# Kernel optimization log

Hardware: AMD Instinct MI355X
Metric: run time of the kernel (lower is better)

The kernel has to match this reference:

```python
import jax, jax.numpy as jnp
import numpy as np

B = 128
GRID = (256, 256)
N = GRID[0] * GRID[1]
P = 1024          # number of persistence pairs per sample (fixed for jit)
T = 512           # landscape sample count
K_MAX = 2
DIMENSIONS = (0, 1)
ADD_T = True


def setup_inputs() -> dict:
    key = jax.random.key(0)
    k1, k2, k3, k4 = jax.random.split(key, 4)
    dtm_val = jax.random.uniform(k1, (B, N), dtype=jnp.float32)
    birth_loc = jax.random.randint(k2, (B, P), 0, N, dtype=jnp.int32)
    death_loc = jax.random.randint(k3, (B, P), 0, N, dtype=jnp.int32)
    ph_dim = jax.random.randint(k4, (B, P), 0, 2, dtype=jnp.int32)
    return {"dtm_val": dtm_val, "birth_loc": birth_loc,
            "death_loc": death_loc, "ph_dim": ph_dim}


def _landscape(dtm_val, birth_loc, death_loc, ph_dim):
    # birth/death filtration values are gathers from the input grid values
    birth = jnp.take_along_axis(dtm_val, birth_loc.astype(jnp.int32), axis=1)  # [B, P]
    death = jnp.take_along_axis(dtm_val, death_loc.astype(jnp.int32), axis=1)  # [B, P]
    unit = jnp.linspace(0.0, 1.0, T, dtype=dtm_val.dtype)                      # [T]

    lands = []
    for d in DIMENSIONS:
        mask = (ph_dim == d)                           # [B, P] pairs of this homology dim
        count = mask.sum(axis=1)                       # [B]
        rank = jnp.cumsum(mask, axis=1) - 1
        mask_k = mask & (rank < K_MAX)                 # first min(count, K_MAX) pairs of this dim
        t_min = jnp.min(jnp.where(mask_k, birth, jnp.inf), axis=1)   # [B]
        t_max = jnp.max(jnp.where(mask_k, death, -jnp.inf), axis=1)  # [B]
        t_min = jnp.where(count > 0, t_min, 0.0)
        t_max = jnp.where(count > 0, t_max, 1.0)
        # adaptive time grid; original gradient treats tseq as constant
        tseq = jax.lax.stop_gradient(
            t_min[:, None] + (t_max - t_min)[:, None] * unit[None, :])        # [B, T]

        # tent functions: [B, T, P]
        fab = jnp.maximum(
            jnp.minimum(tseq[:, :, None] - birth[:, None, :],
                        death[:, None, :] - tseq[:, :, None]),
            0.0)
        fab = jnp.where(mask[:, None, :], fab, 0.0)
        topk, _ = jax.lax.top_k(fab, K_MAX)            # descending sort, take K_MAX: [B, T, K]
        land_d = topk + tseq[:, :, None] if ADD_T else topk
        land_d = jnp.where((count > 0)[:, None, None], land_d, 0.0)
        lands.append(land_d)

    return jnp.stack(lands, axis=1)                    # [B, num_dim, T, K_MAX]


def reference(dtm_val, birth_loc, death_loc, ph_dim):
    return _landscape(dtm_val, birth_loc, death_loc, ph_dim)
```

## Files before the change

kernel.cpp:

```cpp
#include <hip/hip_runtime.h>

constexpr int B_ = 128;
constexpr int N_ = 256 * 256;
constexpr int P_ = 1024;
constexpr int T_ = 512;

__global__ __launch_bounds__(512) void apl_kernel(
    const float* __restrict__ dtm,
    const int*  __restrict__ birth_loc,
    const int*  __restrict__ death_loc,
    const int*  __restrict__ ph_dim,
    float*      __restrict__ out)
{
    const int d   = blockIdx.x;
    const int b   = blockIdx.y;
    const int tid = threadIdx.x;

    __shared__ float2 cbd[P_];
    __shared__ int2   red[512];
    __shared__ int    s_count;
    __shared__ float  s_tmin, s_tmax;

    if (tid == 0) s_count = 0;
    __syncthreads();

    const int*   bl = birth_loc + (size_t)b * P_;
    const int*   dl = death_loc + (size_t)b * P_;
    const int*   pd = ph_dim    + (size_t)b * P_;
    const float* dv = dtm       + (size_t)b * N_;

    const int INF = 0x7fffffff;
    int i1 = INF, i2 = INF;

    #pragma unroll
    for (int r = 0; r < 2; ++r) {
        const int p = tid + r * 512;
        if (pd[p] == d) {
            const float bv = dv[bl[p]];
            const float dvv = dv[dl[p]];
            const int idx = atomicAdd(&s_count, 1);
            cbd[idx] = make_float2(bv, dvv);
            if (i1 == INF) i1 = p; else i2 = p;
        }
    }
    red[tid] = make_int2(i1, i2);
    __syncthreads();

    for (int s = 256; s > 0; s >>= 1) {
        if (tid < s) {
            const int2 a = red[tid];
            const int2 c = red[tid + s];
            const int r1 = min(a.x, c.x);
            const int r2 = min(max(a.x, c.x), min(a.y, c.y));
            red[tid] = make_int2(r1, r2);
        }
        __syncthreads();
    }

    const int cnt = s_count;

    if (tid == 0) {
        float tmin = 0.0f, tmax = 1.0f;
        if (cnt > 0) {
            const int j1 = red[0].x;
            tmin = dv[bl[j1]];
            tmax = dv[dl[j1]];
            if (cnt > 1) {
                const int j2 = red[0].y;
                tmin = fminf(tmin, dv[bl[j2]]);
                tmax = fmaxf(tmax, dv[dl[j2]]);
            }
        }
        s_tmin = tmin; s_tmax = tmax;
    }
    __syncthreads();

    const float tmin = s_tmin, tmax = s_tmax;
    const float ts = tmin + (tmax - tmin) * ((float)tid * (1.0f / (float)(T_ - 1)));

    float a1 = 0.0f, a2 = 0.0f, c1 = 0.0f, c2 = 0.0f;
    int j = 0;
    for (; j + 2 <= cnt; j += 2) {
        const float2 e0 = cbd[j];
        const float2 e1 = cbd[j + 1];
        const float f0 = fmaxf(fminf(ts - e0.x, e0.y - ts), 0.0f);
        const float f1 = fmaxf(fminf(ts - e1.x, e1.y - ts), 0.0f);
        a2 = fmaxf(a2, fminf(a1, f0)); a1 = fmaxf(a1, f0);
        c2 = fmaxf(c2, fminf(c1, f1)); c1 = fmaxf(c1, f1);
    }
    if (j < cnt) {
        const float2 e0 = cbd[j];
        const float f0 = fmaxf(fminf(ts - e0.x, e0.y - ts), 0.0f);
        a2 = fmaxf(a2, fminf(a1, f0)); a1 = fmaxf(a1, f0);
    }
    const float m1 = fmaxf(a1, c1);
    const float m2 = fmaxf(fminf(a1, c1), fmaxf(a2, c2));

    const size_t o = (((size_t)b * 2 + d) * T_ + tid) * 2;
    if (cnt > 0) {
        out[o]     = m1 + ts;
        out[o + 1] = m2 + ts;
    } else {
        out[o]     = 0.0f;
        out[o + 1] = 0.0f;
    }
}

extern "C" void kernel_launch(void* const* d_in, const int* in_sizes, int n_in,
                              void* d_out, int out_size, void* d_ws, size_t ws_size,
                              hipStream_t stream) {
    const float* dtm = (const float*)d_in[0];
    const int*   bl  = (const int*)d_in[1];
    const int*   dl  = (const int*)d_in[2];
    const int*   pd  = (const int*)d_in[3];
    float*       out = (float*)d_out;

    dim3 grid(2, B_);
    dim3 block(512);
    hipLaunchKernelGGL(apl_kernel, grid, block, 0, stream, dtm, bl, dl, pd, out);
}
```

Before: 94.75 us.

## Use ballot-based ordered compaction and split pairs across two threads per sample

```diff
diff --git a/kernel.cpp b/kernel.cpp
--- a/kernel.cpp
+++ b/kernel.cpp
@@ -5,105 +5,102 @@
 constexpr int P_ = 1024;
 constexpr int T_ = 512;
 
-__global__ __launch_bounds__(512) void apl_kernel(
+__device__ __forceinline__ float med3f(float a, float b, float c) {
+    return __builtin_amdgcn_fmed3f(a, b, c);
+}
+
+__global__ __launch_bounds__(1024) void apl_kernel(
     const float* __restrict__ dtm,
     const int*  __restrict__ birth_loc,
     const int*  __restrict__ death_loc,
     const int*  __restrict__ ph_dim,
     float*      __restrict__ out)
 {
-    const int d   = blockIdx.x;
-    const int b   = blockIdx.y;
-    const int tid = threadIdx.x;
+    const int d    = blockIdx.x;
+    const int b    = blockIdx.y;
+    const int tid  = threadIdx.x;
+    const int lane = tid & 63;
+    const int wave = tid >> 6;
 
-    __shared__ float2 cbd[P_];
-    __shared__ int2   red[512];
-    __shared__ int    s_count;
-    __shared__ float  s_tmin, s_tmax;
+    __shared__ float4 sb4[(P_ + 8) / 4];
+    __shared__ float4 sd4[(P_ + 8) / 4];
+    __shared__ int s_wcnt[16];
+    __shared__ int s_wbase[16];
+    __shared__ int s_count;
+    float* sb = (float*)sb4;
+    float* sd = (float*)sd4;
 
-    if (tid == 0) s_count = 0;
-    __syncthreads();
+    sb[tid] = 1e30f;
+    sd[tid] = -1e30f;
+    if (tid < 8) { sb[P_ + tid] = 1e30f; sd[P_ + tid] = -1e30f; }
 
     const int*   bl = birth_loc + (size_t)b * P_;
     const int*   dl = death_loc + (size_t)b * P_;
     const int*   pd = ph_dim    + (size_t)b * P_;
     const float* dv = dtm       + (size_t)b * N_;
 
-    const int INF = 0x7fffffff;
-    int i1 = INF, i2 = INF;
-
-    #pragma unroll
-    for (int r = 0; r < 2; ++r) {
-        const int p = tid + r * 512;
-        if (pd[p] == d) {
-            const float bv = dv[bl[p]];
-            const float dvv = dv[dl[p]];
-            const int idx = atomicAdd(&s_count, 1);
-            cbd[idx] = make_float2(bv, dvv);
-            if (i1 == INF) i1 = p; else i2 = p;
-        }
+    const int pdv = pd[tid];
+    const int bi  = bl[tid];
+    const int di  = dl[tid];
+    const bool m  = (pdv == d);
+    float bv = 0.0f, dvv = 0.0f;
+    if (m) {
+        bv  = dv[bi];
+        dvv = dv[di];
     }
-    red[tid] = make_int2(i1, i2);
+    const unsigned long long mk = __ballot(m);
+    const int prefix = __popcll(mk & ((1ull << lane) - 1ull));
+    if (lane == 0) s_wcnt[wave] = __popcll(mk);
     __syncthreads();
 
-    for (int s = 256; s > 0; s >>= 1) {
-        if (tid < s) {
-            const int2 a = red[tid];
-            const int2 c = red[tid + s];
-            const int r1 = min(a.x, c.x);
-            const int r2 = min(max(a.x, c.x), min(a.y, c.y));
-            red[tid] = make_int2(r1, r2);
-        }
-        __syncthreads();
-    }
-
-    const int cnt = s_count;
-
     if (tid == 0) {
-        float tmin = 0.0f, tmax = 1.0f;
-        if (cnt > 0) {
-            const int j1 = red[0].x;
-            tmin = dv[bl[j1]];
-            tmax = dv[dl[j1]];
-            if (cnt > 1) {
-                const int j2 = red[0].y;
-                tmin = fminf(tmin, dv[bl[j2]]);
-                tmax = fmaxf(tmax, dv[dl[j2]]);
-            }
-        }
-        s_tmin = tmin; s_tmax = tmax;
+        int run = 0;
+        #pragma unroll
+        for (int w = 0; w < 16; ++w) { s_wbase[w] = run; run += s_wcnt[w]; }
+        s_count = run;
     }
     __syncthreads();
 
-    const float tmin = s_tmin, tmax = s_tmax;
-    const float ts = tmin + (tmax - tmin) * ((float)tid * (1.0f / (float)(T_ - 1)));
+    if (m) {
+        const int ix = s_wbase[wave] + prefix;
+        sb[ix] = bv;
+        sd[ix] = dvv;
+    }
+    __syncthreads();
+
+    const int cnt = s_count;
+    float tmin = 0.0f, tmax = 1.0f;
+    if (cnt > 0) {
+        tmin = sb[0]; tmax = sd[0];
+        if (cnt > 1) { tmin = fminf(tmin, sb[1]); tmax = fmaxf(tmax, sd[1]); }
+    }
+
+    const int t = tid >> 1;
+    const int h = tid & 1;
+    const float ts = tmin + (tmax - tmin) * ((float)t * (1.0f / 511.0f));
 
     float a1 = 0.0f, a2 = 0.0f, c1 = 0.0f, c2 = 0.0f;
-    int j = 0;
-    for (; j + 2 <= cnt; j += 2) {
-        const float2 e0 = cbd[j];
-        const float2 e1 = cbd[j + 1];
-        const float f0 = fmaxf(fminf(ts - e0.x, e0.y - ts), 0.0f);
-        const float f1 = fmaxf(fminf(ts - e1.x, e1.y - ts), 0.0f);
-        a2 = fmaxf(a2, fminf(a1, f0)); a1 = fmaxf(a1, f0);
-        c2 = fmaxf(c2, fminf(c1, f1)); c1 = fmaxf(c1, f1);
-    }
-    if (j < cnt) {
-        const float2 e0 = cbd[j];
-        const float f0 = fmaxf(fminf(ts - e0.x, e0.y - ts), 0.0f);
-        a2 = fmaxf(a2, fminf(a1, f0)); a1 = fmaxf(a1, f0);
+    const int kmax = (cnt + 7) >> 3;
+    int idx = h;
+    for (int k = 0; k < kmax; ++k, idx += 2) {
+        const float4 bb = sb4[idx];
+        const float4 dd = sd4[idx];
+        float f;
+        f = fminf(ts - bb.x, dd.x - ts); a2 = med3f(a1, a2, f); a1 = fmaxf(a1, f);
+        f = fminf(ts - bb.y, dd.y - ts); c2 = med3f(c1, c2, f); c1 = fmaxf(c1, f);
+        f = fminf(ts - bb.z, dd.z - ts); a2 = med3f(a1, a2, f); a1 = fmaxf(a1, f);
+        f = fminf(ts - bb.w, dd.w - ts); c2 = med3f(c1, c2, f); c1 = fmaxf(c1, f);
     }
     const float m1 = fmaxf(a1, c1);
     const float m2 = fmaxf(fminf(a1, c1), fmaxf(a2, c2));
+    const float p1 = __shfl_xor(m1, 1);
+    const float p2 = __shfl_xor(m2, 1);
+    const float M1 = fmaxf(m1, p1);
+    const float M2 = fmaxf(fminf(m1, p1), fmaxf(m2, p2));
 
-    const size_t o = (((size_t)b * 2 + d) * T_ + tid) * 2;
-    if (cnt > 0) {
-        out[o]     = m1 + ts;
-        out[o + 1] = m2 + ts;
-    } else {
-        out[o]     = 0.0f;
-        out[o + 1] = 0.0f;
-    }
+    float val = (h == 0) ? M1 : M2;
+    val = (cnt > 0) ? (val + ts) : 0.0f;
+    out[(((size_t)b * 2 + d) * T_ + t) * 2 + h] = val;
 }
 
 extern "C" void kernel_launch(void* const* d_in, const int* in_sizes, int n_in,
@@ -116,6 +113,6 @@
     float*       out = (float*)d_out;
 
     dim3 grid(2, B_);
-    dim3 block(512);
+    dim3 block(1024);
     hipLaunchKernelGGL(apl_kernel, grid, block, 0, stream, dtm, bl, dl, pd, out);
 }
```

Result: faster. 88.35 us (-6.8%).
